# Performance work log

Hardware: AMD Instinct MI355X
Metric: run time of the kernel (lower is better)

## Reference

```python
import jax, jax.numpy as jnp
import numpy as np

NUM_EXPERTS = 8
TOP_K = 2
HIDDEN = 2048
INTER = 1024
B, S = 4, 1024


def setup_inputs() -> dict:
    key = jax.random.key(0)
    ks = jax.random.split(key, 5)
    sx = 1.0 / np.sqrt(HIDDEN)
    si = 1.0 / np.sqrt(INTER)
    return {
        "x": jax.random.normal(ks[0], (B, S, HIDDEN), dtype=jnp.float32),
        # router gate: Linear(hidden -> num_experts), weight stored [E, H] (torch convention)
        "gate_w": jax.random.normal(ks[1], (NUM_EXPERTS, HIDDEN), dtype=jnp.float32) * sx,
        # stacked expert weights: gate/up [E, I, H], down [E, H, I]
        "gate_proj_w": jax.random.normal(ks[2], (NUM_EXPERTS, INTER, HIDDEN), dtype=jnp.float32) * sx,
        "up_proj_w": jax.random.normal(ks[3], (NUM_EXPERTS, INTER, HIDDEN), dtype=jnp.float32) * sx,
        "down_proj_w": jax.random.normal(ks[4], (NUM_EXPERTS, HIDDEN, INTER), dtype=jnp.float32) * si,
    }


def _moe_forward(x, gate_w, gate_proj_w, up_proj_w, down_proj_w):
    Bx, Sx, H = x.shape
    T = Bx * Sx
    h = x.reshape(T, H)
    # --- routing (Qwen3: softmax in fp32, top-k, renormalize) ---
    router_logits = h @ gate_w.T                                   # [T, E]
    probs = jax.nn.softmax(router_logits.astype(jnp.float32), axis=-1)
    top_vals, top_idx = jax.lax.top_k(probs, TOP_K)                # [T, K]
    top_vals = top_vals / jnp.sum(top_vals, axis=-1, keepdims=True)  # norm_topk_prob
    # dense routing weights [T, E]: zero for unselected experts
    rw = jnp.zeros((T, NUM_EXPERTS), dtype=jnp.float32)
    rw = rw.at[jnp.arange(T)[:, None], top_idx].add(top_vals)
    rw = rw.astype(h.dtype)
    # --- SwiGLU experts, computed densely and masked by routing weights ---
    g = jnp.einsum('th,eih->tei', h, gate_proj_w)                  # [T, E, I]
    u = jnp.einsum('th,eih->tei', h, up_proj_w)                    # [T, E, I]
    a = jax.nn.silu(g) * u                                         # [T, E, I]
    out_e = jnp.einsum('tei,ehi->teh', a, down_proj_w)             # [T, E, H]
    out = jnp.einsum('te,teh->th', rw, out_e)                      # [T, H]
    return out.reshape(Bx, Sx, H)


def reference(x, gate_w, gate_proj_w, up_proj_w, down_proj_w):
    return _moe_forward(x, gate_w, gate_proj_w, up_proj_w, down_proj_w)
```

## Files before the change

### kernel.cpp

```cpp
#include <hip/hip_runtime.h>
#include <hip/hip_bf16.h>

#define NUM_EXPERTS 8
#define HIDDEN 2048
#define INTER 1024
#define T_TOKENS 4096

#define BK 32
#define GU_BM 64
#define GU_BN 128
#define DN_BM 64
#define DN_BN 128

typedef __attribute__((ext_vector_type(8))) short short8;
typedef __attribute__((ext_vector_type(8))) unsigned short ushort8_t;
typedef __attribute__((ext_vector_type(4))) float f32x4;

__device__ __forceinline__ ushort f2bf(float f) {
    __hip_bfloat16 h = __float2bfloat16(f);
    return *reinterpret_cast<ushort*>(&h);
}

__device__ __forceinline__ void load_lds16(const void* g, void* lds) {
    __builtin_amdgcn_global_load_lds(
        (const __attribute__((address_space(1))) void*)g,
        (__attribute__((address_space(3))) void*)lds, 16, 0, 0);
}

__global__ __launch_bounds__(256) void cvt_bf16(const float* __restrict__ in,
                                                ushort* __restrict__ out, int n8) {
    int i = blockIdx.x * 256 + threadIdx.x;
    int stride = gridDim.x * 256;
    for (; i < n8; i += stride) {
        const float4* p = (const float4*)in + 2 * (size_t)i;
        float4 a = p[0], b = p[1];
        ushort8_t o;
        o[0] = f2bf(a.x); o[1] = f2bf(a.y); o[2] = f2bf(a.z); o[3] = f2bf(a.w);
        o[4] = f2bf(b.x); o[5] = f2bf(b.y); o[6] = f2bf(b.z); o[7] = f2bf(b.w);
        *((ushort8_t*)out + i) = o;
    }
}

__global__ __launch_bounds__(256) void moe_router(const float* __restrict__ x,
                                                  const float* __restrict__ gw,
                                                  int* __restrict__ top_idx,
                                                  float* __restrict__ top_w,
                                                  int* __restrict__ counts) {
    int wid = threadIdx.x >> 6;
    int lane = threadIdx.x & 63;
    int t = blockIdx.x * 4 + wid;
    if (t >= T_TOKENS) return;
    const float* xt = x + (size_t)t * HIDDEN;
    float acc[NUM_EXPERTS];
#pragma unroll
    for (int e = 0; e < NUM_EXPERTS; e++) acc[e] = 0.f;
    for (int h = lane; h < HIDDEN; h += 64) {
        float xv = xt[h];
#pragma unroll
        for (int e = 0; e < NUM_EXPERTS; e++)
            acc[e] = fmaf(xv, gw[e * HIDDEN + h], acc[e]);
    }
#pragma unroll
    for (int e = 0; e < NUM_EXPERTS; e++) {
#pragma unroll
        for (int off = 32; off > 0; off >>= 1)
            acc[e] += __shfl_xor(acc[e], off);
    }
    if (lane == 0) {
        int i1 = 0; float l1 = acc[0];
#pragma unroll
        for (int e = 1; e < NUM_EXPERTS; e++)
            if (acc[e] > l1) { l1 = acc[e]; i1 = e; }
        int i2 = -1; float l2 = -3.4e38f;
#pragma unroll
        for (int e = 0; e < NUM_EXPERTS; e++)
            if (e != i1 && acc[e] > l2) { l2 = acc[e]; i2 = e; }
        float w2 = __expf(l2 - l1);
        float denom = 1.f + w2;
        top_idx[t * 2 + 0] = i1;
        top_idx[t * 2 + 1] = i2;
        top_w[t * 2 + 0] = 1.f / denom;
        top_w[t * 2 + 1] = w2 / denom;
        atomicAdd(&counts[i1], 1);
        atomicAdd(&counts[i2], 1);
    }
}

__global__ void moe_offsets(const int* __restrict__ counts,
                            int* __restrict__ ebase, int* __restrict__ cursor) {
    if (threadIdx.x == 0 && blockIdx.x == 0) {
        int s = 0;
        for (int e = 0; e < NUM_EXPERTS; e++) {
            ebase[e] = s; cursor[e] = s; s += counts[e];
        }
    }
}

__global__ __launch_bounds__(256) void moe_scatter(const int* __restrict__ top_idx,
                                                   int* __restrict__ cursor,
                                                   int* __restrict__ slot_tok,
                                                   int* __restrict__ inv_slot) {
    int t = blockIdx.x * 256 + threadIdx.x;
    if (t >= T_TOKENS) return;
#pragma unroll
    for (int k = 0; k < 2; k++) {
        int e = top_idx[t * 2 + k];
        int pos = atomicAdd(&cursor[e], 1);
        slot_tok[pos] = t;
        inv_slot[t * 2 + k] = pos;
    }
}

__global__ __launch_bounds__(256, 4) void moe_gateup(const ushort* __restrict__ xb,
                                                     const ushort* __restrict__ wgb,
                                                     const ushort* __restrict__ wub,
                                                     const int* __restrict__ slot_tok,
                                                     const int* __restrict__ ebase,
                                                     const int* __restrict__ ecnt,
                                                     ushort* __restrict__ act) {
    __shared__ ushort ldsA[2][GU_BM * BK];
    __shared__ ushort ldsG[2][GU_BN * BK];
    __shared__ ushort ldsU[2][GU_BN * BK];

    const int wg = blockIdx.x;
    const int wgid = (wg & 7) * 512 + (wg >> 3);
    const int e = wgid >> 9;
    const int rem = wgid & 511;
    const int bm = rem & 63;
    const int bn = rem >> 6;

    const int cnt = ecnt[e];
    if (bm * GU_BM >= cnt) return;
    const int b0 = ebase[e];

    const int tid = threadIdx.x;
    const int lane = tid & 63;
    const int wid = tid >> 6;
    const int wr = wid >> 1, wc = wid & 1;

    const int r = tid >> 2, cs = tid & 3;
    const int scl = (cs ^ ((r >> 1) & 3)) * 8;
    const int ar = bm * GU_BM + r;
    const int tok = slot_tok[b0 + ((ar < cnt) ? ar : (cnt - 1))];
    const ushort* pA = xb + (size_t)tok * HIDDEN + scl;
    const size_t wrow0 = (size_t)e * INTER + (size_t)(bn * GU_BN + r);
    const ushort* pG0 = wgb + wrow0 * HIDDEN + scl;
    const ushort* pG1 = pG0 + (size_t)64 * HIDDEN;
    const ushort* pU0 = wub + wrow0 * HIDDEN + scl;
    const ushort* pU1 = pU0 + (size_t)64 * HIDDEN;

    const int fr = lane & 15;
    const int colsw = (((lane >> 4) ^ ((fr >> 1) & 3)) * 8);

    f32x4 accg[2][4] = {};
    f32x4 accu[2][4] = {};

#define GU_STAGE(buf, t)                                              \
    do {                                                              \
        const int _o = (t) * BK;                                      \
        load_lds16(pA + _o,  &ldsA[buf][tid * 8]);                    \
        load_lds16(pG0 + _o, &ldsG[buf][tid * 8]);                    \
        load_lds16(pG1 + _o, &ldsG[buf][2048 + tid * 8]);             \
        load_lds16(pU0 + _o, &ldsU[buf][tid * 8]);                    \
        load_lds16(pU1 + _o, &ldsU[buf][2048 + tid * 8]);             \
    } while (0)

#define GU_FRAGS_MFMA(cur)                                            \
    do {                                                              \
        const ushort* LA = ldsA[cur];                                 \
        const ushort* LG = ldsG[cur];                                 \
        const ushort* LU = ldsU[cur];                                 \
        short8 a[2], bg[4], bu[4];                                    \
        _Pragma("unroll")                                             \
        for (int m = 0; m < 2; m++)                                   \
            a[m] = *(const short8*)(LA + (wr * 32 + m * 16 + fr) * BK + colsw); \
        _Pragma("unroll")                                             \
        for (int n = 0; n < 4; n++) {                                 \
            bg[n] = *(const short8*)(LG + (wc * 64 + n * 16 + fr) * BK + colsw); \
            bu[n] = *(const short8*)(LU + (wc * 64 + n * 16 + fr) * BK + colsw); \
        }                                                             \
        asm volatile("s_waitcnt lgkmcnt(0)" ::: "memory");            \
        asm volatile("s_barrier" ::: "memory");                       \
        if (t + 2 < NT) GU_STAGE(cur, t + 2);                         \
        _Pragma("unroll")                                             \
        for (int m = 0; m < 2; m++) {                                 \
            _Pragma("unroll")                                         \
            for (int n = 0; n < 4; n++) {                             \
                accg[m][n] = __builtin_amdgcn_mfma_f32_16x16x32_bf16(a[m], bg[n], accg[m][n], 0, 0, 0); \
                accu[m][n] = __builtin_amdgcn_mfma_f32_16x16x32_bf16(a[m], bu[n], accu[m][n], 0, 0, 0); \
            }                                                         \
        }                                                             \
    } while (0)

    const int NT = HIDDEN / BK;
    GU_STAGE(0, 0);
    GU_STAGE(1, 1);

    for (int t = 0; t < NT - 1; ++t) {
        asm volatile("s_waitcnt vmcnt(5)" ::: "memory");
        asm volatile("s_barrier" ::: "memory");
        const int cur = t & 1;
        GU_FRAGS_MFMA(cur);
    }
    {
        const int t = NT - 1;
        asm volatile("s_waitcnt vmcnt(0)" ::: "memory");
        asm volatile("s_barrier" ::: "memory");
        const int cur = t & 1;
        GU_FRAGS_MFMA(cur);
    }
#undef GU_FRAGS_MFMA
#undef GU_STAGE

#pragma unroll
    for (int m = 0; m < 2; m++) {
#pragma unroll
        for (int rr = 0; rr < 4; rr++) {
            int row = bm * GU_BM + wr * 32 + m * 16 + (lane >> 4) * 4 + rr;
            if (row < cnt) {
                size_t arow = (size_t)(b0 + row) * INTER;
#pragma unroll
                for (int n = 0; n < 4; n++) {
                    int col = bn * GU_BN + wc * 64 + n * 16 + fr;
                    float g = accg[m][n][rr];
                    float u = accu[m][n][rr];
                    float s = g / (1.f + __expf(-g));
                    act[arow + col] = f2bf(s * u);
                }
            }
        }
    }
}

__global__ __launch_bounds__(256, 6) void moe_down(const ushort* __restrict__ act,
                                                   const ushort* __restrict__ wdb,
                                                   const int* __restrict__ ebase,
                                                   const int* __restrict__ ecnt,
                                                   float* __restrict__ out_e) {
    __shared__ ushort ldsA[2][DN_BM * BK];
    __shared__ ushort ldsB[2][DN_BN * BK];

    const int wg = blockIdx.x;
    const int wgid = (wg & 7) * 1024 + (wg >> 3);
    const int e = wgid >> 10;
    const int rem = wgid & 1023;
    const int bm = rem & 63;
    const int bn = rem >> 6;

    const int cnt = ecnt[e];
    if (bm * DN_BM >= cnt) return;
    const int b0 = ebase[e];

    const int tid = threadIdx.x;
    const int lane = tid & 63;
    const int wid = tid >> 6;
    const int wr = wid >> 1, wc = wid & 1;

    const int r = tid >> 2, cs = tid & 3;
    const int scl = (cs ^ ((r >> 1) & 3)) * 8;
    const int ar = bm * DN_BM + r;
    const int sr = b0 + ((ar < cnt) ? ar : (cnt - 1));
    const ushort* pA = act + (size_t)sr * INTER + scl;
    const size_t wrow = (size_t)e * HIDDEN + (size_t)(bn * DN_BN + r);
    const ushort* pB0 = wdb + wrow * INTER + scl;
    const ushort* pB1 = pB0 + (size_t)64 * INTER;

    const int fr = lane & 15;
    const int colsw = (((lane >> 4) ^ ((fr >> 1) & 3)) * 8);

    f32x4 acc[2][4] = {};

#define DN_STAGE(buf, t)                                              \
    do {                                                              \
        const int _o = (t) * BK;                                      \
        load_lds16(pA + _o,  &ldsA[buf][tid * 8]);                    \
        load_lds16(pB0 + _o, &ldsB[buf][tid * 8]);                    \
        load_lds16(pB1 + _o, &ldsB[buf][2048 + tid * 8]);             \
    } while (0)

#define DN_FRAGS_MFMA(cur)                                            \
    do {                                                              \
        const ushort* LA = ldsA[cur];                                 \
        const ushort* LB = ldsB[cur];                                 \
        short8 a[2], b[4];                                            \
        _Pragma("unroll")                                             \
        for (int m = 0; m < 2; m++)                                   \
            a[m] = *(const short8*)(LA + (wr * 32 + m * 16 + fr) * BK + colsw); \
        _Pragma("unroll")                                             \
        for (int n = 0; n < 4; n++)                                   \
            b[n] = *(const short8*)(LB + (wc * 64 + n * 16 + fr) * BK + colsw); \
        asm volatile("s_waitcnt lgkmcnt(0)" ::: "memory");            \
        asm volatile("s_barrier" ::: "memory");                       \
        if (t + 2 < NT) DN_STAGE(cur, t + 2);                         \
        _Pragma("unroll")                                             \
        for (int m = 0; m < 2; m++) {                                 \
            _Pragma("unroll")                                         \
            for (int n = 0; n < 4; n++)                               \
                acc[m][n] = __builtin_amdgcn_mfma_f32_16x16x32_bf16(a[m], b[n], acc[m][n], 0, 0, 0); \
        }                                                             \
    } while (0)

    const int NT = INTER / BK;
    DN_STAGE(0, 0);
    DN_STAGE(1, 1);

    for (int t = 0; t < NT - 1; ++t) {
        asm volatile("s_waitcnt vmcnt(3)" ::: "memory");
        asm volatile("s_barrier" ::: "memory");
        const int cur = t & 1;
        DN_FRAGS_MFMA(cur);
    }
    {
        const int t = NT - 1;
        asm volatile("s_waitcnt vmcnt(0)" ::: "memory");
        asm volatile("s_barrier" ::: "memory");
        const int cur = t & 1;
        DN_FRAGS_MFMA(cur);
    }
#undef DN_FRAGS_MFMA
#undef DN_STAGE

#pragma unroll
    for (int m = 0; m < 2; m++) {
#pragma unroll
        for (int rr = 0; rr < 4; rr++) {
            int row = bm * DN_BM + wr * 32 + m * 16 + (lane >> 4) * 4 + rr;
            if (row < cnt) {
                float* orow = out_e + (size_t)(b0 + row) * HIDDEN;
#pragma unroll
                for (int n = 0; n < 4; n++) {
                    int col = bn * DN_BN + wc * 64 + n * 16 + fr;
                    orow[col] = acc[m][n][rr];
                }
            }
        }
    }
}

__global__ __launch_bounds__(256) void moe_gather(const float* __restrict__ out_e,
                                                  const int* __restrict__ inv_slot,
                                                  const float* __restrict__ top_w,
                                                  float* __restrict__ out) {
    int t = blockIdx.x;
    int c = threadIdx.x * 8;
    int s0 = inv_slot[t * 2 + 0], s1 = inv_slot[t * 2 + 1];
    float w0 = top_w[t * 2 + 0], w1 = top_w[t * 2 + 1];
    const float4* r0 = (const float4*)(out_e + (size_t)s0 * HIDDEN + c);
    const float4* r1 = (const float4*)(out_e + (size_t)s1 * HIDDEN + c);
    float4* po = (float4*)(out + (size_t)t * HIDDEN + c);
#pragma unroll
    for (int j = 0; j < 2; j++) {
        float4 a = r0[j], b = r1[j], o;
        o.x = w0 * a.x + w1 * b.x;
        o.y = w0 * a.y + w1 * b.y;
        o.z = w0 * a.z + w1 * b.z;
        o.w = w0 * a.w + w1 * b.w;
        po[j] = o;
    }
}

extern "C" void kernel_launch(void* const* d_in, const int* in_sizes, int n_in,
                              void* d_out, int out_size, void* d_ws, size_t ws_size,
                              hipStream_t stream) {
    const float* x  = (const float*)d_in[0];
    const float* gw = (const float*)d_in[1];
    const float* wg = (const float*)d_in[2];
    const float* wu = (const float*)d_in[3];
    const float* wd = (const float*)d_in[4];
    float* out = (float*)d_out;

    char* ws = (char*)d_ws;
    ushort* xb  = (ushort*)(ws);
    ushort* wgb = (ushort*)(ws + (16u << 20));
    ushort* wub = (ushort*)(ws + (48u << 20));
    ushort* wdb = (ushort*)(ws + (80u << 20));
    ushort* act = (ushort*)(ws + (112u << 20));
    float* out_e = (float*)(ws);
    char* p = ws + (128u << 20);
    int*   top_idx  = (int*)p;   p += 32768;
    float* top_w    = (float*)p; p += 32768;
    int*   slot_tok = (int*)p;   p += 32768;
    int*   inv_slot = (int*)p;   p += 32768;
    int*   counts   = (int*)p;   p += 128;
    int*   ebase    = (int*)p;   p += 128;
    int*   cursor   = (int*)p;   p += 128;

    hipMemsetAsync(counts, 0, 128, stream);

    cvt_bf16<<<1024, 256, 0, stream>>>(x,  xb,  (T_TOKENS * HIDDEN) / 8);
    cvt_bf16<<<1024, 256, 0, stream>>>(wg, wgb, (NUM_EXPERTS * INTER * HIDDEN) / 8);
    cvt_bf16<<<1024, 256, 0, stream>>>(wu, wub, (NUM_EXPERTS * INTER * HIDDEN) / 8);
    cvt_bf16<<<1024, 256, 0, stream>>>(wd, wdb, (NUM_EXPERTS * HIDDEN * INTER) / 8);

    moe_router<<<T_TOKENS / 4, 256, 0, stream>>>(x, gw, top_idx, top_w, counts);
    moe_offsets<<<1, 64, 0, stream>>>(counts, ebase, cursor);
    moe_scatter<<<(T_TOKENS + 255) / 256, 256, 0, stream>>>(top_idx, cursor, slot_tok, inv_slot);

    moe_gateup<<<4096, 256, 0, stream>>>(xb, wgb, wub, slot_tok, ebase, counts, act);
    moe_down<<<8192, 256, 0, stream>>>(act, wdb, ebase, counts, out_e);
    moe_gather<<<T_TOKENS, 256, 0, stream>>>(out_e, inv_slot, top_w, out);
}
```

Baseline: 600.7 us.

## Enlarge gate/up and down GEMM tiles and fuse bf16 conversion launches

Doubles the token tile of the gate/up GEMM to 128 rows and grows the down GEMM tile to 128x256, so each warp computes 4x4 or 4x8 MFMA fragments. The staging, wait counts, grid decode and launch sizes are adjusted to match. This raises reuse of each LDS-staged weight tile and cuts redundant weight traffic, at the cost of more registers, lower occupancy (launch bounds drop to 2 blocks) and more padding waste on partially filled expert tiles. The four separate fp32-to-bf16 conversion launches are merged into one 2D-grid launch to reduce launch overhead.

```diff
diff --git a/kernel.cpp b/kernel.cpp
--- a/kernel.cpp
+++ b/kernel.cpp
@@ -7,10 +7,10 @@
 #define T_TOKENS 4096
 
 #define BK 32
-#define GU_BM 64
+#define GU_BM 128
 #define GU_BN 128
-#define DN_BM 64
-#define DN_BN 128
+#define DN_BM 128
+#define DN_BN 256
 
 typedef __attribute__((ext_vector_type(8))) short short8;
 typedef __attribute__((ext_vector_type(8))) unsigned short ushort8_t;
@@ -27,8 +27,17 @@
         (__attribute__((address_space(3))) void*)lds, 16, 0, 0);
 }
 
-__global__ __launch_bounds__(256) void cvt_bf16(const float* __restrict__ in,
-                                                ushort* __restrict__ out, int n8) {
+__global__ __launch_bounds__(256) void cvt_all(const float* __restrict__ x,  ushort* __restrict__ xb,
+                                               const float* __restrict__ wg, ushort* __restrict__ wgb,
+                                               const float* __restrict__ wu, ushort* __restrict__ wub,
+                                               const float* __restrict__ wd, ushort* __restrict__ wdb) {
+    const float* in; ushort* out; int n8;
+    switch (blockIdx.y) {
+        case 0:  in = x;  out = xb;  n8 = (T_TOKENS * HIDDEN) / 8; break;
+        case 1:  in = wg; out = wgb; n8 = (NUM_EXPERTS * INTER * HIDDEN) / 8; break;
+        case 2:  in = wu; out = wub; n8 = (NUM_EXPERTS * INTER * HIDDEN) / 8; break;
+        default: in = wd; out = wdb; n8 = (NUM_EXPERTS * HIDDEN * INTER) / 8; break;
+    }
     int i = blockIdx.x * 256 + threadIdx.x;
     int stride = gridDim.x * 256;
     for (; i < n8; i += stride) {
@@ -111,7 +120,7 @@
     }
 }
 
-__global__ __launch_bounds__(256, 4) void moe_gateup(const ushort* __restrict__ xb,
+__global__ __launch_bounds__(256, 2) void moe_gateup(const ushort* __restrict__ xb,
                                                      const ushort* __restrict__ wgb,
                                                      const ushort* __restrict__ wub,
                                                      const int* __restrict__ slot_tok,
@@ -123,11 +132,11 @@
     __shared__ ushort ldsU[2][GU_BN * BK];
 
     const int wg = blockIdx.x;
-    const int wgid = (wg & 7) * 512 + (wg >> 3);
-    const int e = wgid >> 9;
-    const int rem = wgid & 511;
-    const int bm = rem & 63;
-    const int bn = rem >> 6;
+    const int wgid = (wg & 7) * 256 + (wg >> 3);
+    const int e = wgid >> 8;
+    const int rem = wgid & 255;
+    const int bm = rem & 31;
+    const int bn = rem >> 5;
 
     const int cnt = ecnt[e];
     if (bm * GU_BM >= cnt) return;
@@ -140,9 +149,12 @@
 
     const int r = tid >> 2, cs = tid & 3;
     const int scl = (cs ^ ((r >> 1) & 3)) * 8;
-    const int ar = bm * GU_BM + r;
-    const int tok = slot_tok[b0 + ((ar < cnt) ? ar : (cnt - 1))];
-    const ushort* pA = xb + (size_t)tok * HIDDEN + scl;
+    const int ar0 = bm * GU_BM + r;
+    const int ar1 = ar0 + 64;
+    const int tok0 = slot_tok[b0 + ((ar0 < cnt) ? ar0 : (cnt - 1))];
+    const int tok1 = slot_tok[b0 + ((ar1 < cnt) ? ar1 : (cnt - 1))];
+    const ushort* pA0 = xb + (size_t)tok0 * HIDDEN + scl;
+    const ushort* pA1 = xb + (size_t)tok1 * HIDDEN + scl;
     const size_t wrow0 = (size_t)e * INTER + (size_t)(bn * GU_BN + r);
     const ushort* pG0 = wgb + wrow0 * HIDDEN + scl;
     const ushort* pG1 = pG0 + (size_t)64 * HIDDEN;
@@ -152,13 +164,14 @@
     const int fr = lane & 15;
     const int colsw = (((lane >> 4) ^ ((fr >> 1) & 3)) * 8);
 
-    f32x4 accg[2][4] = {};
-    f32x4 accu[2][4] = {};
+    f32x4 accg[4][4] = {};
+    f32x4 accu[4][4] = {};
 
 #define GU_STAGE(buf, t)                                              \
     do {                                                              \
         const int _o = (t) * BK;                                      \
-        load_lds16(pA + _o,  &ldsA[buf][tid * 8]);                    \
+        load_lds16(pA0 + _o, &ldsA[buf][tid * 8]);                    \
+        load_lds16(pA1 + _o, &ldsA[buf][2048 + tid * 8]);             \
         load_lds16(pG0 + _o, &ldsG[buf][tid * 8]);                    \
         load_lds16(pG1 + _o, &ldsG[buf][2048 + tid * 8]);             \
         load_lds16(pU0 + _o, &ldsU[buf][tid * 8]);                    \
@@ -170,10 +183,10 @@
         const ushort* LA = ldsA[cur];                                 \
         const ushort* LG = ldsG[cur];                                 \
         const ushort* LU = ldsU[cur];                                 \
-        short8 a[2], bg[4], bu[4];                                    \
-        _Pragma("unroll")                                             \
-        for (int m = 0; m < 2; m++)                                   \
-            a[m] = *(const short8*)(LA + (wr * 32 + m * 16 + fr) * BK + colsw); \
+        short8 a[4], bg[4], bu[4];                                    \
+        _Pragma("unroll")                                             \
+        for (int m = 0; m < 4; m++)                                   \
+            a[m] = *(const short8*)(LA + (wr * 64 + m * 16 + fr) * BK + colsw); \
         _Pragma("unroll")                                             \
         for (int n = 0; n < 4; n++) {                                 \
             bg[n] = *(const short8*)(LG + (wc * 64 + n * 16 + fr) * BK + colsw); \
@@ -183,7 +196,7 @@
         asm volatile("s_barrier" ::: "memory");                       \
         if (t + 2 < NT) GU_STAGE(cur, t + 2);                         \
         _Pragma("unroll")                                             \
-        for (int m = 0; m < 2; m++) {                                 \
+        for (int m = 0; m < 4; m++) {                                 \
             _Pragma("unroll")                                         \
             for (int n = 0; n < 4; n++) {                             \
                 accg[m][n] = __builtin_amdgcn_mfma_f32_16x16x32_bf16(a[m], bg[n], accg[m][n], 0, 0, 0); \
@@ -197,7 +210,7 @@
     GU_STAGE(1, 1);
 
     for (int t = 0; t < NT - 1; ++t) {
-        asm volatile("s_waitcnt vmcnt(5)" ::: "memory");
+        asm volatile("s_waitcnt vmcnt(6)" ::: "memory");
         asm volatile("s_barrier" ::: "memory");
         const int cur = t & 1;
         GU_FRAGS_MFMA(cur);
@@ -213,10 +226,10 @@
 #undef GU_STAGE
 
 #pragma unroll
-    for (int m = 0; m < 2; m++) {
+    for (int m = 0; m < 4; m++) {
 #pragma unroll
         for (int rr = 0; rr < 4; rr++) {
-            int row = bm * GU_BM + wr * 32 + m * 16 + (lane >> 4) * 4 + rr;
+            int row = bm * GU_BM + wr * 64 + m * 16 + (lane >> 4) * 4 + rr;
             if (row < cnt) {
                 size_t arow = (size_t)(b0 + row) * INTER;
 #pragma unroll
@@ -232,7 +245,7 @@
     }
 }
 
-__global__ __launch_bounds__(256, 6) void moe_down(const ushort* __restrict__ act,
+__global__ __launch_bounds__(256, 2) void moe_down(const ushort* __restrict__ act,
                                                    const ushort* __restrict__ wdb,
                                                    const int* __restrict__ ebase,
                                                    const int* __restrict__ ecnt,
@@ -241,11 +254,11 @@
     __shared__ ushort ldsB[2][DN_BN * BK];
 
     const int wg = blockIdx.x;
-    const int wgid = (wg & 7) * 1024 + (wg >> 3);
-    const int e = wgid >> 10;
-    const int rem = wgid & 1023;
-    const int bm = rem & 63;
-    const int bn = rem >> 6;
+    const int wgid = (wg & 7) * 256 + (wg >> 3);
+    const int e = wgid >> 8;
+    const int rem = wgid & 255;
+    const int bm = rem & 31;
+    const int bn = rem >> 5;
 
     const int cnt = ecnt[e];
     if (bm * DN_BM >= cnt) return;
@@ -258,44 +271,52 @@
 
     const int r = tid >> 2, cs = tid & 3;
     const int scl = (cs ^ ((r >> 1) & 3)) * 8;
-    const int ar = bm * DN_BM + r;
-    const int sr = b0 + ((ar < cnt) ? ar : (cnt - 1));
-    const ushort* pA = act + (size_t)sr * INTER + scl;
+    const int ar0 = bm * DN_BM + r;
+    const int ar1 = ar0 + 64;
+    const int sr0 = b0 + ((ar0 < cnt) ? ar0 : (cnt - 1));
+    const int sr1 = b0 + ((ar1 < cnt) ? ar1 : (cnt - 1));
+    const ushort* pA0 = act + (size_t)sr0 * INTER + scl;
+    const ushort* pA1 = act + (size_t)sr1 * INTER + scl;
     const size_t wrow = (size_t)e * HIDDEN + (size_t)(bn * DN_BN + r);
     const ushort* pB0 = wdb + wrow * INTER + scl;
     const ushort* pB1 = pB0 + (size_t)64 * INTER;
+    const ushort* pB2 = pB0 + (size_t)128 * INTER;
+    const ushort* pB3 = pB0 + (size_t)192 * INTER;
 
     const int fr = lane & 15;
     const int colsw = (((lane >> 4) ^ ((fr >> 1) & 3)) * 8);
 
-    f32x4 acc[2][4] = {};
+    f32x4 acc[4][8] = {};
 
 #define DN_STAGE(buf, t)                                              \
     do {                                                              \
         const int _o = (t) * BK;                                      \
-        load_lds16(pA + _o,  &ldsA[buf][tid * 8]);                    \
+        load_lds16(pA0 + _o, &ldsA[buf][tid * 8]);                    \
+        load_lds16(pA1 + _o, &ldsA[buf][2048 + tid * 8]);             \
         load_lds16(pB0 + _o, &ldsB[buf][tid * 8]);                    \
         load_lds16(pB1 + _o, &ldsB[buf][2048 + tid * 8]);             \
+        load_lds16(pB2 + _o, &ldsB[buf][4096 + tid * 8]);             \
+        load_lds16(pB3 + _o, &ldsB[buf][6144 + tid * 8]);             \
     } while (0)
 
 #define DN_FRAGS_MFMA(cur)                                            \
     do {                                                              \
         const ushort* LA = ldsA[cur];                                 \
         const ushort* LB = ldsB[cur];                                 \
-        short8 a[2], b[4];                                            \
-        _Pragma("unroll")                                             \
-        for (int m = 0; m < 2; m++)                                   \
-            a[m] = *(const short8*)(LA + (wr * 32 + m * 16 + fr) * BK + colsw); \
-        _Pragma("unroll")                                             \
-        for (int n = 0; n < 4; n++)                                   \
-            b[n] = *(const short8*)(LB + (wc * 64 + n * 16 + fr) * BK + colsw); \
+        short8 a[4], b[8];                                            \
+        _Pragma("unroll")                                             \
+        for (int m = 0; m < 4; m++)                                   \
+            a[m] = *(const short8*)(LA + (wr * 64 + m * 16 + fr) * BK + colsw); \
+        _Pragma("unroll")                                             \
+        for (int n = 0; n < 8; n++)                                   \
+            b[n] = *(const short8*)(LB + (wc * 128 + n * 16 + fr) * BK + colsw); \
         asm volatile("s_waitcnt lgkmcnt(0)" ::: "memory");            \
         asm volatile("s_barrier" ::: "memory");                       \
         if (t + 2 < NT) DN_STAGE(cur, t + 2);                         \
         _Pragma("unroll")                                             \
-        for (int m = 0; m < 2; m++) {                                 \
+        for (int m = 0; m < 4; m++) {                                 \
             _Pragma("unroll")                                         \
-            for (int n = 0; n < 4; n++)                               \
+            for (int n = 0; n < 8; n++)                               \
                 acc[m][n] = __builtin_amdgcn_mfma_f32_16x16x32_bf16(a[m], b[n], acc[m][n], 0, 0, 0); \
         }                                                             \
     } while (0)
@@ -305,7 +326,7 @@
     DN_STAGE(1, 1);
 
     for (int t = 0; t < NT - 1; ++t) {
-        asm volatile("s_waitcnt vmcnt(3)" ::: "memory");
+        asm volatile("s_waitcnt vmcnt(6)" ::: "memory");
         asm volatile("s_barrier" ::: "memory");
         const int cur = t & 1;
         DN_FRAGS_MFMA(cur);
@@ -321,15 +342,15 @@
 #undef DN_STAGE
 
 #pragma unroll
-    for (int m = 0; m < 2; m++) {
+    for (int m = 0; m < 4; m++) {
 #pragma unroll
         for (int rr = 0; rr < 4; rr++) {
-            int row = bm * DN_BM + wr * 32 + m * 16 + (lane >> 4) * 4 + rr;
+            int row = bm * DN_BM + wr * 64 + m * 16 + (lane >> 4) * 4 + rr;
             if (row < cnt) {
                 float* orow = out_e + (size_t)(b0 + row) * HIDDEN;
 #pragma unroll
-                for (int n = 0; n < 4; n++) {
-                    int col = bn * DN_BN + wc * 64 + n * 16 + fr;
+                for (int n = 0; n < 8; n++) {
+                    int col = bn * DN_BN + wc * 128 + n * 16 + fr;
                     orow[col] = acc[m][n][rr];
                 }
             }
@@ -387,16 +408,13 @@
 
     hipMemsetAsync(counts, 0, 128, stream);
 
-    cvt_bf16<<<1024, 256, 0, stream>>>(x,  xb,  (T_TOKENS * HIDDEN) / 8);
-    cvt_bf16<<<1024, 256, 0, stream>>>(wg, wgb, (NUM_EXPERTS * INTER * HIDDEN) / 8);
-    cvt_bf16<<<1024, 256, 0, stream>>>(wu, wub, (NUM_EXPERTS * INTER * HIDDEN) / 8);
-    cvt_bf16<<<1024, 256, 0, stream>>>(wd, wdb, (NUM_EXPERTS * HIDDEN * INTER) / 8);
+    cvt_all<<<dim3(768, 4), 256, 0, stream>>>(x, xb, wg, wgb, wu, wub, wd, wdb);
 
     moe_router<<<T_TOKENS / 4, 256, 0, stream>>>(x, gw, top_idx, top_w, counts);
     moe_offsets<<<1, 64, 0, stream>>>(counts, ebase, cursor);
     moe_scatter<<<(T_TOKENS + 255) / 256, 256, 0, stream>>>(top_idx, cursor, slot_tok, inv_slot);
 
-    moe_gateup<<<4096, 256, 0, stream>>>(xb, wgb, wub, slot_tok, ebase, counts, act);
-    moe_down<<<8192, 256, 0, stream>>>(act, wdb, ebase, counts, out_e);
+    moe_gateup<<<2048, 256, 0, stream>>>(xb, wgb, wub, slot_tok, ebase, counts, act);
+    moe_down<<<2048, 256, 0, stream>>>(act, wdb, ebase, counts, out_e);
     moe_gather<<<T_TOKENS, 256, 0, stream>>>(out_e, inv_slot, top_w, out);
 }
```

Result: no change. 596.3 us (-0.7%).
